# Performance work log

Measured on AMD Instinct MI355X. Metric: run time of the kernel, lower is better.

Reference implementation:

```python
import jax, jax.numpy as jnp
import numpy as np

B, T, D, H = 16, 2048, 512, 512


def setup_inputs() -> dict:
    key = jax.random.key(0)
    k1, k2, k3, k4, k5, k6 = jax.random.split(key, 6)
    s = 1.0 / np.sqrt(H)  # PyTorch RNN init scale
    return {
        "input_features": jax.random.normal(k1, (B, T, D), jnp.float32),
        "start_index": jax.random.randint(k2, (B,), 0, T),
        "w_ih": jax.random.uniform(k3, (3 * H, D), jnp.float32, -s, s),
        "w_hh": jax.random.uniform(k4, (3 * H, H), jnp.float32, -s, s),
        "b_ih": jax.random.uniform(k5, (3 * H,), jnp.float32, -s, s),
        "b_hh": jax.random.uniform(k6, (3 * H,), jnp.float32, -s, s),
    }


def reference(input_features, start_index, w_ih, w_hh, b_ih, b_hh):
    # Faithful to RNNSeqMaskEncoder._forward_residual with 1-layer uni GRU,
    # Identity residual (input_dim == hidden_dim), default_hidden == zeros.
    Bn, Tn, _ = input_features.shape
    Hn = w_hh.shape[1]
    dt = input_features.dtype
    # Precompute input projections for all timesteps: (B, T, 3H)
    x_proj = jnp.einsum('btd,gd->btg', input_features, w_ih) + b_ih
    # Mask at step i: keep hidden only if start_index < i (else reset to zeros).
    masks = (start_index[None, :] < jnp.arange(Tn)[:, None]).astype(dt)  # (T, B)

    def step(h, inp):
        xg, m = inp                     # xg: (B, 3H), m: (B,)
        h = h * m[:, None]              # mask-based hidden reset
        hg = h @ w_hh.T + b_hh          # (B, 3H)
        xr, xz, xn = jnp.split(xg, 3, axis=-1)
        hr, hz, hn = jnp.split(hg, 3, axis=-1)
        r = jax.nn.sigmoid(xr + hr)
        z = jax.nn.sigmoid(xz + hz)
        n = jnp.tanh(xn + r * hn)
        h_new = (1.0 - z) * n + z * h   # PyTorch GRU update
        return h_new, h_new

    h0 = jnp.zeros((Bn, Hn), dt)
    _, hs = jax.lax.scan(step, h0, (x_proj.transpose(1, 0, 2), masks))  # hs: (T, B, H)
    hidden_seq = hs.transpose(1, 0, 2)          # (B, T, H)
    output = input_features + hidden_seq        # residual (Identity linear)
    hidden = hidden_seq[None]                   # (n_layers*dirs=1, B, T, H)
    return output, hidden
```

## Files before the change

### kernel.cpp

```cpp
#include <hip/hip_runtime.h>
#include <cstdint>

typedef short bf16x8 __attribute__((ext_vector_type(8)));
typedef float f32x4  __attribute__((ext_vector_type(4)));
typedef unsigned u32x4 __attribute__((ext_vector_type(4)));

constexpr int Bn = 16, Tn = 2048, Dn = 512, Hn = 512;
constexpr int NWG = 16, JWG = 32, NTH = 512;
constexpr int NLAUNCH = 128;
constexpr int TC1 = 16;

#define MFMA16(a, b, c) __builtin_amdgcn_mfma_f32_16x16x32_bf16((a), (b), (c), 0, 0, 0)

#define POLLS_FAST() do { \
  asm volatile("global_load_dwordx4 %0, %1, off sc0 nt" : "=v"(a0) : "v"(hpF)      : "memory"); \
  asm volatile("global_load_dwordx4 %0, %1, off sc0 nt" : "=v"(a1) : "v"(hpF + 16) : "memory"); \
  asm volatile("global_load_dwordx4 %0, %1, off sc0 nt" : "=v"(a2) : "v"(hpF + 32) : "memory"); \
  asm volatile("global_load_dwordx4 %0, %1, off sc0 nt" : "=v"(a3) : "v"(hpF + 48) : "memory"); \
} while (0)
#define POLLS_SLOW() do { \
  asm volatile("global_load_dwordx4 %0, %1, off sc0 sc1" : "=v"(a0) : "v"(hpS)      : "memory"); \
  asm volatile("global_load_dwordx4 %0, %1, off sc0 sc1" : "=v"(a1) : "v"(hpS + 16) : "memory"); \
  asm volatile("global_load_dwordx4 %0, %1, off sc0 sc1" : "=v"(a2) : "v"(hpS + 32) : "memory"); \
  asm volatile("global_load_dwordx4 %0, %1, off sc0 sc1" : "=v"(a3) : "v"(hpS + 48) : "memory"); \
} while (0)
#define PUBS_PEND(slot_t) do { \
  if (!(jj & 1)) { \
    unsigned* dstS_ = ringS + (size_t)((slot_t) & 1) * (Bn * Hn / 2) + ((bq * Hn + jg) >> 1); \
    asm volatile("global_store_dword %0, %1, off sc0 sc1" :: "v"(dstS_), "v"(pendP) : "memory"); \
  } \
} while (0)

__device__ __forceinline__ unsigned short f2bf(float f) {
  union { float f; unsigned u; } v; v.f = f;
  unsigned r = v.u + 0x7FFFu + ((v.u >> 16) & 1u);
  return (unsigned short)(r >> 16);
}
__device__ __forceinline__ float lo2f(unsigned u) { union { unsigned u; float f; } v; v.u = u << 16;        return v.f; }
__device__ __forceinline__ float hi2f(unsigned u) { union { unsigned u; float f; } v; v.u = u & 0xFFFF0000u; return v.f; }
__device__ __forceinline__ float asf(unsigned u)  { union { unsigned u; float f; } v; v.u = u; return v.f; }
__device__ __forceinline__ unsigned asu(float f)  { union { float f; unsigned u; } v; v.f = f; return v.u; }

__global__ __launch_bounds__(NTH, 2) void xproj_pass(
    const float* __restrict__ x, const float* __restrict__ w_ih,
    const float* __restrict__ b_ih, const float* __restrict__ b_hh,
    unsigned* __restrict__ xrz, unsigned short* __restrict__ xnb)
{
  const int tid = threadIdx.x, lane = tid & 63, wv = tid >> 6;
  const int kw = wv & 3, jw = wv >> 2;
  const int arow = lane & 15, koff = (lane >> 4) * 8;
  const int wg = blockIdx.x, t0 = blockIdx.y * TC1;
  const int kb = kw * 128;

  bf16x8 wif[3][4];
  #pragma unroll
  for (int g = 0; g < 3; ++g) {
    const int grow = g * Hn + wg * JWG + jw * 16 + arow;
    #pragma unroll
    for (int s = 0; s < 4; ++s) {
      const float* pi = w_ih + (size_t)grow * Dn + kb + s * 32 + koff;
      bf16x8 b;
      #pragma unroll
      for (int i = 0; i < 8; ++i) b[i] = (short)f2bf(pi[i]);
      wif[g][s] = b;
    }
  }
  const int bq = tid >> 5, jj = tid & 31, jg = wg * JWG + jj;
  const float br = b_ih[jg]          + b_hh[jg];
  const float bz = b_ih[Hn + jg]     + b_hh[Hn + jg];
  const float bn = b_ih[2 * Hn + jg];

  __shared__ float red[3][4][16][32];
  const float* xrow = x + (size_t)arow * Tn * Dn + kb + koff;

  for (int tt = 0; tt < TC1; ++tt) {
    const int t = t0 + tt;
    const float* xt = xrow + (size_t)t * Dn;
    f32x4 xa[4][2];
    #pragma unroll
    for (int s = 0; s < 4; ++s) {
      xa[s][0] = *(const f32x4*)(xt + s * 32);
      xa[s][1] = *(const f32x4*)(xt + s * 32 + 4);
    }
    bf16x8 xf[4];
    #pragma unroll
    for (int s = 0; s < 4; ++s) {
      unsigned d0, d1, d2, d3;
      asm("v_cvt_pk_bf16_f32 %0, %1, %2" : "=v"(d0) : "v"(xa[s][0][0]), "v"(xa[s][0][1]));
      asm("v_cvt_pk_bf16_f32 %0, %1, %2" : "=v"(d1) : "v"(xa[s][0][2]), "v"(xa[s][0][3]));
      asm("v_cvt_pk_bf16_f32 %0, %1, %2" : "=v"(d2) : "v"(xa[s][1][0]), "v"(xa[s][1][1]));
      asm("v_cvt_pk_bf16_f32 %0, %1, %2" : "=v"(d3) : "v"(xa[s][1][2]), "v"(xa[s][1][3]));
      union { u32x4 u; bf16x8 v; } xu;
      xu.u[0] = d0; xu.u[1] = d1; xu.u[2] = d2; xu.u[3] = d3;
      xf[s] = xu.v;
    }
    f32x4 ar = {0,0,0,0}, az = {0,0,0,0}, an = {0,0,0,0};
    #pragma unroll
    for (int s = 0; s < 4; ++s) {
      ar = MFMA16(xf[s], wif[0][s], ar);
      az = MFMA16(xf[s], wif[1][s], az);
      an = MFMA16(xf[s], wif[2][s], an);
    }
    #pragma unroll
    for (int i = 0; i < 4; ++i) {
      const int r_ = (lane >> 4) * 4 + i, c_ = jw * 16 + (lane & 15);
      red[0][kw][r_][c_] = ar[i];
      red[1][kw][r_][c_] = az[i];
      red[2][kw][r_][c_] = an[i];
    }
    __syncthreads();
    float sr = br, sz = bz, sn = bn;
    #pragma unroll
    for (int k2 = 0; k2 < 4; ++k2) {
      sr += red[0][k2][bq][jj];
      sz += red[1][k2][bq][jj];
      sn += red[2][k2][bq][jj];
    }
    unsigned rz;
    asm("v_cvt_pk_bf16_f32 %0, %1, %2" : "=v"(rz) : "v"(sr), "v"(sz));
    const size_t o = (size_t)(wg * Tn + t) * 512 + tid;
    xrz[o] = rz;
    xnb[o] = f2bf(sn);
    __syncthreads();
  }
}

template<bool XP>
__global__ __launch_bounds__(NTH, 2) void gru_scan(
    const float* __restrict__ x, const int* __restrict__ start,
    const float* __restrict__ w_ih, const float* __restrict__ w_hh,
    const float* __restrict__ b_ih, const float* __restrict__ b_hh,
    float* __restrict__ out, unsigned* __restrict__ ectl,
    unsigned* __restrict__ ringF, unsigned* __restrict__ ringS,
    const unsigned* __restrict__ xrz, const unsigned short* __restrict__ xnb)
{
  __shared__ int s_rank;
  __shared__ int s_fastok;
  if (threadIdx.x == 0) {
    unsigned xcc;
    asm volatile("s_getreg_b32 %0, hwreg(HW_REG_XCC_ID)" : "=s"(xcc));
    xcc &= 7u;
    if (blockIdx.x == 0)
      __hip_atomic_store(&ectl[8], xcc | 0x100u, __ATOMIC_RELAXED, __HIP_MEMORY_SCOPE_AGENT);
    unsigned w;
    while ((((w = __hip_atomic_load(&ectl[8], __ATOMIC_RELAXED, __HIP_MEMORY_SCOPE_AGENT))) & 0x100u) == 0u)
      __builtin_amdgcn_s_sleep(2);
    if ((w & 7u) != xcc)
      for (int i = 0; i < 800; ++i) __builtin_amdgcn_s_sleep(2);
    const unsigned slot =
        __hip_atomic_fetch_add(&ectl[9], 1u, __ATOMIC_RELAXED, __HIP_MEMORY_SCOPE_AGENT);
    s_rank = (slot < (unsigned)NWG) ? (int)slot : -1;
  }
  __syncthreads();
  const int rank = s_rank;
  if (rank < 0) return;

  const int tid = threadIdx.x, lane = tid & 63, wv = tid >> 6;
  const int kw = wv & 3, jw = wv >> 2;
  const int arow = lane & 15, koff = (lane >> 4) * 8;
  const int kb = kw * 128;
  constexpr int NG = XP ? 3 : 4;

  bf16x8 whf[3][4], wif[3][4];
  #pragma unroll
  for (int g = 0; g < 3; ++g) {
    const int grow = g * Hn + rank * JWG + jw * 16 + arow;
    #pragma unroll
    for (int s = 0; s < 4; ++s) {
      const float* ph = w_hh + (size_t)grow * Dn + kb + s * 32 + koff;
      bf16x8 a;
      #pragma unroll
      for (int i = 0; i < 8; ++i) a[i] = (short)f2bf(ph[i]);
      whf[g][s] = a;
      if constexpr (!XP) {
        const float* pi = w_ih + (size_t)grow * Dn + kb + s * 32 + koff;
        bf16x8 b;
        #pragma unroll
        for (int i = 0; i < 8; ++i) b[i] = (short)f2bf(pi[i]);
        wif[g][s] = b;
      }
    }
  }

  if (threadIdx.x == 0) {
    if (rank == 0) {
      const unsigned* tp = &ectl[32];
      asm volatile("global_store_dword %0, %1, off" :: "v"(tp), "v"(0xA5A5A5A5u) : "memory");
      asm volatile("s_waitcnt vmcnt(0)" ::: "memory");
      __hip_atomic_store(&ectl[10], 1u, __ATOMIC_RELAXED, __HIP_MEMORY_SCOPE_AGENT);
    }
    while (__hip_atomic_load(&ectl[10], __ATOMIC_RELAXED, __HIP_MEMORY_SCOPE_AGENT) == 0u)
      __builtin_amdgcn_s_sleep(1);
    int ok = 0;
    const unsigned* tp = &ectl[32];
    for (int i = 0; i < 1024 && !ok; ++i) {
      unsigned tok;
      asm volatile("global_load_dword %0, %1, off sc0 nt" : "=v"(tok) : "v"(tp) : "memory");
      asm volatile("s_waitcnt vmcnt(0)" ::: "memory");
      ok = (tok == 0xA5A5A5A5u);
      if (!ok && (i & 15) == 15) __builtin_amdgcn_s_sleep(1);
    }
    s_fastok = ok;
    __hip_atomic_store(&ectl[64 + rank], 1u, __ATOMIC_RELAXED, __HIP_MEMORY_SCOPE_AGENT);
    for (;;) {
      unsigned rdy = 0;
      for (int i = 0; i < 16; ++i)
        rdy += __hip_atomic_load(&ectl[64 + i], __ATOMIC_RELAXED, __HIP_MEMORY_SCOPE_AGENT);
      if (rdy == 16u) break;
      __builtin_amdgcn_s_sleep(1);
    }
  }
  __syncthreads();
  bool fastwave = (s_fastok != 0);

  const int bq = tid >> 5, jj = tid & 31, jg = rank * JWG + jj;
  const float bias_nh = b_hh[2 * Hn + jg];
  float bias_r = 0.f, bias_z = 0.f, bias_nx = 0.f;
  if constexpr (!XP) {
    bias_r  = b_ih[jg]      + b_hh[jg];
    bias_z  = b_ih[Hn + jg] + b_hh[Hn + jg];
    bias_nx = b_ih[2 * Hn + jg];
  }
  const int start_g = start[bq];
  const int start_a = start[arow];
  const int jwr  = jj >> 4;
  const int lsrc = ((bq >> 2) << 4) | (jj & 15);
  const int ib   = bq & 3;

  float h_own = 0.f;
  unsigned po0u = 0u, po1u = 0u;
  unsigned pendP = 0u;
  __shared__ float red[2][NG][4][2][64][4];

  const float*          xres_p = x   + (size_t)bq * Tn * Dn + jg;
  const unsigned*       xrz_p  = xrz + (size_t)rank * Tn * 512 + tid;
  const unsigned short* xn_p   = xnb + (size_t)rank * Tn * 512 + tid;
  const float*          xrow   = x   + (size_t)arow * Tn * Dn + kb + koff;

  unsigned prz0=0, prz1=0, prz2=0, prz3=0, pn0=0, pn1=0, pn2=0, pn3=0;
  unsigned pxr0=0, pxr1=0, pxr2=0, pxr3=0;
  f32x4 xa0[4][2], xa1[4][2]; float xr0 = 0.f, xr1 = 0.f;
  if constexpr (XP) {
    prz0 = xrz_p[0];   pn0 = xn_p[0];
    prz1 = xrz_p[512]; pn1 = xn_p[512];
    pxr0 = asu(xres_p[0]); pxr1 = asu(xres_p[Dn]);
  } else {
    #pragma unroll
    for (int s = 0; s < 4; ++s) {
      xa0[s][0] = *(const f32x4*)(xrow + s * 32);
      xa0[s][1] = *(const f32x4*)(xrow + s * 32 + 4);
      xa1[s][0] = *(const f32x4*)(xrow + (size_t)Dn + s * 32);
      xa1[s][1] = *(const f32x4*)(xrow + (size_t)Dn + s * 32 + 4);
    }
    xr0 = xres_p[0]; xr1 = xres_p[Dn];
  }

  auto step = [&](int t, unsigned& crz, unsigned& cn, unsigned& cxr,
                  unsigned& frz, unsigned& fn, unsigned& fxr,
                  f32x4 (&xa)[4][2], float& xr) {
    const bool hv = (t > 0);
    const float xres_t = XP ? asf(cxr) : xr;
    f32x4 ar = {0,0,0,0}, az = {0,0,0,0}, anx = {0,0,0,0}, anh = {0,0,0,0};

    if constexpr (!XP) {
      bf16x8 xf[4];
      #pragma unroll
      for (int s = 0; s < 4; ++s) {
        unsigned d0, d1, d2, d3;
        asm("v_cvt_pk_bf16_f32 %0, %1, %2" : "=v"(d0) : "v"(xa[s][0][0]), "v"(xa[s][0][1]));
        asm("v_cvt_pk_bf16_f32 %0, %1, %2" : "=v"(d1) : "v"(xa[s][0][2]), "v"(xa[s][0][3]));
        asm("v_cvt_pk_bf16_f32 %0, %1, %2" : "=v"(d2) : "v"(xa[s][1][0]), "v"(xa[s][1][1]));
        asm("v_cvt_pk_bf16_f32 %0, %1, %2" : "=v"(d3) : "v"(xa[s][1][2]), "v"(xa[s][1][3]));
        union { u32x4 u; bf16x8 v; } xu;
        xu.u[0] = d0; xu.u[1] = d1; xu.u[2] = d2; xu.u[3] = d3;
        xf[s] = xu.v;
      }
      #pragma unroll
      for (int s = 0; s < 4; ++s) {
        ar  = MFMA16(xf[s], wif[0][s], ar);
        az  = MFMA16(xf[s], wif[1][s], az);
        anx = MFMA16(xf[s], wif[2][s], anx);
      }
    }

    const size_t off_h = (size_t)(t & 1) * (Bn * Hn / 2) + ((arow * Hn + kb + koff) >> 1);
    const unsigned* hpF = ringF + off_h;
    const unsigned* hpS = ringS + off_h;
    u32x4 a0, a1, a2, a3;
    if (hv) {
      if (!fastwave) PUBS_PEND(t);
      if (fastwave) POLLS_FAST(); else POLLS_SLOW();
      asm volatile("s_waitcnt vmcnt(0)" ::: "memory");
      __builtin_amdgcn_sched_barrier(0);
      const unsigned pexp = (unsigned)((t >> 1) & 1);
      int tries = 0;
      for (;;) {
        int ok;
        if (pexp) {
          const unsigned andv = a0[0] & a0[1] & a0[2] & a0[3] & a1[0] & a1[1] & a1[2] & a1[3]
                              & a2[0] & a2[1] & a2[2] & a2[3] & a3[0] & a3[1] & a3[2] & a3[3];
          ok = ((andv & 0x00010001u) == 0x00010001u);
        } else {
          const unsigned orv  = a0[0] | a0[1] | a0[2] | a0[3] | a1[0] | a1[1] | a1[2] | a1[3]
                              | a2[0] | a2[1] | a2[2] | a2[3] | a3[0] | a3[1] | a3[2] | a3[3];
          ok = ((orv & 0x00010001u) == 0u);
        }
        if (__all(ok)) break;
        ++tries;
        if (fastwave && tries >= 8192) {
          fastwave = false;
          PUBS_PEND(t);
        }
        if (!fastwave || tries > 32) __builtin_amdgcn_s_sleep(1);
        if (fastwave) POLLS_FAST(); else POLLS_SLOW();
        asm volatile("s_waitcnt vmcnt(0)" ::: "memory");
        __builtin_amdgcn_sched_barrier(0);
      }
    }

    if (hv) {
      const bool am = (start_a < t);
      union { u32x4 u; bf16x8 v; } c0, c1, c2, c3;
      const u32x4 zz = {0, 0, 0, 0};
      c0.u = am ? a0 : zz; c1.u = am ? a1 : zz; c2.u = am ? a2 : zz; c3.u = am ? a3 : zz;
      ar  = MFMA16(c0.v, whf[0][0], ar);  az  = MFMA16(c0.v, whf[1][0], az);
      anh = MFMA16(c0.v, whf[2][0], anh);
      ar  = MFMA16(c1.v, whf[0][1], ar);  az  = MFMA16(c1.v, whf[1][1], az);
      anh = MFMA16(c1.v, whf[2][1], anh);
      ar  = MFMA16(c2.v, whf[0][2], ar);  az  = MFMA16(c2.v, whf[1][2], az);
      anh = MFMA16(c2.v, whf[2][2], anh);
      ar  = MFMA16(c3.v, whf[0][3], ar);  az  = MFMA16(c3.v, whf[1][3], az);
      anh = MFMA16(c3.v, whf[2][3], anh);
    }

    const int par = t & 1;
    *(f32x4*)&red[par][0][kw][jw][lane][0] = ar;
    *(f32x4*)&red[par][1][kw][jw][lane][0] = az;
    if constexpr (XP) {
      *(f32x4*)&red[par][2][kw][jw][lane][0] = anh;
    } else {
      *(f32x4*)&red[par][2][kw][jw][lane][0] = anx;
      *(f32x4*)&red[par][3][kw][jw][lane][0] = anh;
    }
    __syncthreads();

    if constexpr (XP) {
      const int tf = (t + 2 < Tn) ? t + 2 : Tn - 1;
      const unsigned*       p1 = xrz_p + (size_t)tf * 512;
      const unsigned short* p2 = xn_p  + (size_t)tf * 512;
      const float*          p3 = xres_p + (size_t)tf * Dn;
      asm volatile("global_load_dword  %0, %1, off" : "=v"(frz) : "v"(p1) : "memory");
      asm volatile("global_load_ushort %0, %1, off" : "=v"(fn)  : "v"(p2) : "memory");
      asm volatile("global_load_dword  %0, %1, off" : "=v"(fxr) : "v"(p3) : "memory");
    } else {
      const int tf = (t + 2 < Tn) ? t + 2 : Tn - 1;
      const float* xt = xrow + (size_t)tf * Dn;
      #pragma unroll
      for (int s = 0; s < 4; ++s) {
        xa[s][0] = *(const f32x4*)(xt + s * 32);
        xa[s][1] = *(const f32x4*)(xt + s * 32 + 4);
      }
      xr = xres_p[(size_t)tf * Dn];
    }
    if (hv) {
      const size_t poo = ((size_t)bq * Tn + (t - 1)) * Hn + jg;
      const float* q0 = out + poo;
      const float* q1 = out + (size_t)Bn * Tn * Hn + poo;
      asm volatile("global_store_dword %0, %1, off" :: "v"(q0), "v"(po0u) : "memory");
      asm volatile("global_store_dword %0, %1, off" :: "v"(q1), "v"(po1u) : "memory");
    }
    if (hv && fastwave) PUBS_PEND(t);

    float sr, sz, snx, snh;
    if constexpr (XP) { sr = lo2f(crz); sz = hi2f(crz); snx = lo2f(cn); snh = bias_nh; }
    else              { sr = bias_r;    sz = bias_z;    snx = bias_nx;  snh = bias_nh; }
    #pragma unroll
    for (int k2 = 0; k2 < 4; ++k2) {
      sr += red[par][0][k2][jwr][lsrc][ib];
      sz += red[par][1][k2][jwr][lsrc][ib];
      if constexpr (XP) {
        snh += red[par][2][k2][jwr][lsrc][ib];
      } else {
        snx += red[par][2][k2][jwr][lsrc][ib];
        snh += red[par][3][k2][jwr][lsrc][ib];
      }
    }
    const float r  = 1.f / (1.f + __expf(-sr));
    const float z  = 1.f / (1.f + __expf(-sz));
    const float ea = __expf(2.f * (snx + r * snh));
    const float n  = 1.f - 2.f / (ea + 1.f);
    const float hm = (start_g < t) ? h_own : 0.f;
    const float hn = (1.f - z) * n + z * hm;
    h_own = hn;

    const unsigned ptag01 = (unsigned)(((t + 1) >> 1) & 1) * 0x00010001u;
    const float hpart = asf((unsigned)__shfl_xor((int)asu(hn), 1, 64));
    unsigned packed;
    asm("v_cvt_pk_bf16_f32 %0, %1, %2" : "=v"(packed) : "v"(hn), "v"(hpart));
    packed = (packed & 0xFFFEFFFEu) | ptag01;
    if (!(jj & 1)) {
      unsigned* dstF = ringF + (size_t)((t + 1) & 1) * (Bn * Hn / 2) + ((bq * Hn + jg) >> 1);
      asm volatile("global_store_dword %0, %1, off" :: "v"(dstF), "v"(packed) : "memory");
    }
    pendP = packed;

    po0u = asu(xres_t + hn);
    po1u = asu(hn);
  };

  #pragma unroll 1
  for (int t = 0; t < Tn; t += 4) {
    step(t + 0, prz0, pn0, pxr0, prz2, pn2, pxr2, xa0, xr0);
    step(t + 1, prz1, pn1, pxr1, prz3, pn3, pxr3, xa1, xr1);
    step(t + 2, prz2, pn2, pxr2, prz0, pn0, pxr0, xa0, xr0);
    step(t + 3, prz3, pn3, pxr3, prz1, pn1, pxr1, xa1, xr1);
  }
  {
    const size_t poo = ((size_t)bq * Tn + (Tn - 1)) * Hn + jg;
    out[poo] = asf(po0u);
    out[(size_t)Bn * Tn * Hn + poo] = asf(po1u);
  }
}

extern "C" void kernel_launch(void* const* d_in, const int* in_sizes, int n_in,
                              void* d_out, int out_size, void* d_ws, size_t ws_size,
                              hipStream_t stream) {
  const float* x     = (const float*)d_in[0];
  const int*   start = (const int*)d_in[1];
  const float* w_ih  = (const float*)d_in[2];
  const float* w_hh  = (const float*)d_in[3];
  const float* b_ih  = (const float*)d_in[4];
  const float* b_hh  = (const float*)d_in[5];
  float* out = (float*)d_out;

  unsigned* ectl  = (unsigned*)d_ws;
  unsigned* ringF = (unsigned*)((char*)d_ws + 4096);
  unsigned* ringS = (unsigned*)((char*)d_ws + 36864);
  const size_t xrz_off   = 131072;
  const size_t xrz_bytes = (size_t)NWG * Tn * 512 * 4;
  const size_t xn_bytes  = (size_t)NWG * Tn * 512 * 2;
  unsigned*       xrz = (unsigned*)((char*)d_ws + xrz_off);
  unsigned short* xnb = (unsigned short*)((char*)d_ws + xrz_off + xrz_bytes);
  const bool xp = ws_size >= xrz_off + xrz_bytes + xn_bytes;

  hipMemsetAsync(d_ws, 0x00, 4096, stream);
  hipMemsetAsync((char*)d_ws + 4096,  0x00, 16384, stream);
  hipMemsetAsync((char*)d_ws + 20480, 0x01, 16384, stream);
  hipMemsetAsync((char*)d_ws + 36864, 0x00, 16384, stream);
  hipMemsetAsync((char*)d_ws + 53248, 0x01, 16384, stream);
  if (xp) {
    hipLaunchKernelGGL(xproj_pass, dim3(NWG, Tn / TC1), dim3(NTH), 0, stream,
                       x, w_ih, b_ih, b_hh, xrz, xnb);
    hipLaunchKernelGGL(gru_scan<true>, dim3(NLAUNCH), dim3(NTH), 0, stream,
                       x, start, w_ih, w_hh, b_ih, b_hh, out, ectl, ringF, ringS, xrz, xnb);
  } else {
    hipLaunchKernelGGL(gru_scan<false>, dim3(NLAUNCH), dim3(NTH), 0, stream,
                       x, start, w_ih, w_hh, b_ih, b_hh, out, ectl, ringF, ringS,
                       (const unsigned*)d_ws, (const unsigned short*)d_ws);
  }
}
```

Baseline: 5.262 ms.

## Agree on fast path globally, reorder stores, and swizzle LDS reduction layout

All workgroups now agree once at startup whether the fast coherent ring path works, using an AND over per-rank flags. This replaces the per-wave fallback that republished to the slow ring, and each step now writes to exactly one ring. The output stores move ahead of the poll wait, which now waits with vmcnt(2) so the stores can stay in flight, and the MFMA and reduction block moves after the next-step prefetch loads. The LDS reduction buffer is laid out as [batch][column] with an XOR swizzle so reads are simple and avoid bank conflicts. The trade-off is the loss of a runtime fallback if the fast path stalls mid-run, which risks a hang.

Result: faster. 4.693 ms (-10.8%).

```diff
diff --git a/kernel.cpp b/kernel.cpp
--- a/kernel.cpp
+++ b/kernel.cpp
@@ -24,12 +24,6 @@
   asm volatile("global_load_dwordx4 %0, %1, off sc0 sc1" : "=v"(a2) : "v"(hpS + 32) : "memory"); \
   asm volatile("global_load_dwordx4 %0, %1, off sc0 sc1" : "=v"(a3) : "v"(hpS + 48) : "memory"); \
 } while (0)
-#define PUBS_PEND(slot_t) do { \
-  if (!(jj & 1)) { \
-    unsigned* dstS_ = ringS + (size_t)((slot_t) & 1) * (Bn * Hn / 2) + ((bq * Hn + jg) >> 1); \
-    asm volatile("global_store_dword %0, %1, off sc0 sc1" :: "v"(dstS_), "v"(pendP) : "memory"); \
-  } \
-} while (0)
 
 __device__ __forceinline__ unsigned short f2bf(float f) {
   union { float f; unsigned u; } v; v.f = f;
@@ -135,7 +129,7 @@
     const unsigned* __restrict__ xrz, const unsigned short* __restrict__ xnb)
 {
   __shared__ int s_rank;
-  __shared__ int s_fastok;
+  __shared__ int s_fast;
   if (threadIdx.x == 0) {
     unsigned xcc;
     asm volatile("s_getreg_b32 %0, hwreg(HW_REG_XCC_ID)" : "=s"(xcc));
@@ -200,18 +194,23 @@
       ok = (tok == 0xA5A5A5A5u);
       if (!ok && (i & 15) == 15) __builtin_amdgcn_s_sleep(1);
     }
-    s_fastok = ok;
-    __hip_atomic_store(&ectl[64 + rank], 1u, __ATOMIC_RELAXED, __HIP_MEMORY_SCOPE_AGENT);
+    __hip_atomic_store(&ectl[64 + rank], ok ? 1u : 2u, __ATOMIC_RELAXED, __HIP_MEMORY_SCOPE_AGENT);
+    unsigned andok;
     for (;;) {
-      unsigned rdy = 0;
-      for (int i = 0; i < 16; ++i)
-        rdy += __hip_atomic_load(&ectl[64 + i], __ATOMIC_RELAXED, __HIP_MEMORY_SCOPE_AGENT);
-      if (rdy == 16u) break;
+      andok = 1u;
+      unsigned done = 0;
+      for (int i = 0; i < 16; ++i) {
+        const unsigned v = __hip_atomic_load(&ectl[64 + i], __ATOMIC_RELAXED, __HIP_MEMORY_SCOPE_AGENT);
+        done += (v != 0u);
+        andok &= (v == 1u);
+      }
+      if (done == 16u) break;
       __builtin_amdgcn_s_sleep(1);
     }
+    s_fast = (int)andok;
   }
   __syncthreads();
-  bool fastwave = (s_fastok != 0);
+  const bool fast = (s_fast != 0);
 
   const int bq = tid >> 5, jj = tid & 31, jg = rank * JWG + jj;
   const float bias_nh = b_hh[2 * Hn + jg];
@@ -223,14 +222,11 @@
   }
   const int start_g = start[bq];
   const int start_a = start[arow];
-  const int jwr  = jj >> 4;
-  const int lsrc = ((bq >> 2) << 4) | (jj & 15);
-  const int ib   = bq & 3;
+  const int jr = jj ^ (((bq >> 2) & 1) << 4);
 
   float h_own = 0.f;
   unsigned po0u = 0u, po1u = 0u;
-  unsigned pendP = 0u;
-  __shared__ float red[2][NG][4][2][64][4];
+  __shared__ float red[2][NG][4][16][32];
 
   const float*          xres_p = x   + (size_t)bq * Tn * Dn + jg;
   const unsigned*       xrz_p  = xrz + (size_t)rank * Tn * 512 + tid;
@@ -288,9 +284,16 @@
     const unsigned* hpS = ringS + off_h;
     u32x4 a0, a1, a2, a3;
     if (hv) {
-      if (!fastwave) PUBS_PEND(t);
-      if (fastwave) POLLS_FAST(); else POLLS_SLOW();
-      asm volatile("s_waitcnt vmcnt(0)" ::: "memory");
+      if (fast) POLLS_FAST(); else POLLS_SLOW();
+      {
+        const size_t poo = ((size_t)bq * Tn + (t - 1)) * Hn + jg;
+        const float* q0 = out + poo;
+        const float* q1 = out + (size_t)Bn * Tn * Hn + poo;
+        asm volatile("global_store_dword %0, %1, off" :: "v"(q0), "v"(po0u) : "memory");
+        asm volatile("global_store_dword %0, %1, off" :: "v"(q1), "v"(po1u) : "memory");
+      }
+      if (fast) { asm volatile("s_waitcnt vmcnt(2)" ::: "memory"); }
+      else      { asm volatile("s_waitcnt vmcnt(0)" ::: "memory"); }
       __builtin_amdgcn_sched_barrier(0);
       const unsigned pexp = (unsigned)((t >> 1) & 1);
       int tries = 0;
@@ -307,42 +310,12 @@
         }
         if (__all(ok)) break;
         ++tries;
-        if (fastwave && tries >= 8192) {
-          fastwave = false;
-          PUBS_PEND(t);
-        }
-        if (!fastwave || tries > 32) __builtin_amdgcn_s_sleep(1);
-        if (fastwave) POLLS_FAST(); else POLLS_SLOW();
+        if (!fast || tries > 32) __builtin_amdgcn_s_sleep(1);
+        if (fast) POLLS_FAST(); else POLLS_SLOW();
         asm volatile("s_waitcnt vmcnt(0)" ::: "memory");
         __builtin_amdgcn_sched_barrier(0);
       }
     }
-
-    if (hv) {
-      const bool am = (start_a < t);
-      union { u32x4 u; bf16x8 v; } c0, c1, c2, c3;
-      const u32x4 zz = {0, 0, 0, 0};
-      c0.u = am ? a0 : zz; c1.u = am ? a1 : zz; c2.u = am ? a2 : zz; c3.u = am ? a3 : zz;
-      ar  = MFMA16(c0.v, whf[0][0], ar);  az  = MFMA16(c0.v, whf[1][0], az);
-      anh = MFMA16(c0.v, whf[2][0], anh);
-      ar  = MFMA16(c1.v, whf[0][1], ar);  az  = MFMA16(c1.v, whf[1][1], az);
-      anh = MFMA16(c1.v, whf[2][1], anh);
-      ar  = MFMA16(c2.v, whf[0][2], ar);  az  = MFMA16(c2.v, whf[1][2], az);
-      anh = MFMA16(c2.v, whf[2][2], anh);
-      ar  = MFMA16(c3.v, whf[0][3], ar);  az  = MFMA16(c3.v, whf[1][3], az);
-      anh = MFMA16(c3.v, whf[2][3], anh);
-    }
-
-    const int par = t & 1;
-    *(f32x4*)&red[par][0][kw][jw][lane][0] = ar;
-    *(f32x4*)&red[par][1][kw][jw][lane][0] = az;
-    if constexpr (XP) {
-      *(f32x4*)&red[par][2][kw][jw][lane][0] = anh;
-    } else {
-      *(f32x4*)&red[par][2][kw][jw][lane][0] = anx;
-      *(f32x4*)&red[par][3][kw][jw][lane][0] = anh;
-    }
-    __syncthreads();
 
     if constexpr (XP) {
       const int tf = (t + 2 < Tn) ? t + 2 : Tn - 1;
@@ -362,27 +335,49 @@
       }
       xr = xres_p[(size_t)tf * Dn];
     }
+
     if (hv) {
-      const size_t poo = ((size_t)bq * Tn + (t - 1)) * Hn + jg;
-      const float* q0 = out + poo;
-      const float* q1 = out + (size_t)Bn * Tn * Hn + poo;
-      asm volatile("global_store_dword %0, %1, off" :: "v"(q0), "v"(po0u) : "memory");
-      asm volatile("global_store_dword %0, %1, off" :: "v"(q1), "v"(po1u) : "memory");
-    }
-    if (hv && fastwave) PUBS_PEND(t);
-
+      const bool am = (start_a < t);
+      union { u32x4 u; bf16x8 v; } c0, c1, c2, c3;
+      const u32x4 zz = {0, 0, 0, 0};
+      c0.u = am ? a0 : zz; c1.u = am ? a1 : zz; c2.u = am ? a2 : zz; c3.u = am ? a3 : zz;
+      ar  = MFMA16(c0.v, whf[0][0], ar);  az  = MFMA16(c0.v, whf[1][0], az);
+      anh = MFMA16(c0.v, whf[2][0], anh);
+      ar  = MFMA16(c1.v, whf[0][1], ar);  az  = MFMA16(c1.v, whf[1][1], az);
+      anh = MFMA16(c1.v, whf[2][1], anh);
+      ar  = MFMA16(c2.v, whf[0][2], ar);  az  = MFMA16(c2.v, whf[1][2], az);
+      anh = MFMA16(c2.v, whf[2][2], anh);
+      ar  = MFMA16(c3.v, whf[0][3], ar);  az  = MFMA16(c3.v, whf[1][3], az);
+      anh = MFMA16(c3.v, whf[2][3], anh);
+    }
+
+    const int par = t & 1;
+    #pragma unroll
+    for (int i = 0; i < 4; ++i) {
+      const int r_ = (lane >> 4) * 4 + i;
+      const int c_ = (jw * 16 + (lane & 15)) ^ (((lane >> 4) & 1) << 4);
+      red[par][0][kw][r_][c_] = ar[i];
+      red[par][1][kw][r_][c_] = az[i];
+      if constexpr (XP) {
+        red[par][2][kw][r_][c_] = anh[i];
+      } else {
+        red[par][2][kw][r_][c_] = anx[i];
+        red[par][3][kw][r_][c_] = anh[i];
+      }
+    }
+    __syncthreads();
     float sr, sz, snx, snh;
     if constexpr (XP) { sr = lo2f(crz); sz = hi2f(crz); snx = lo2f(cn); snh = bias_nh; }
     else              { sr = bias_r;    sz = bias_z;    snx = bias_nx;  snh = bias_nh; }
     #pragma unroll
     for (int k2 = 0; k2 < 4; ++k2) {
-      sr += red[par][0][k2][jwr][lsrc][ib];
-      sz += red[par][1][k2][jwr][lsrc][ib];
+      sr += red[par][0][k2][bq][jr];
+      sz += red[par][1][k2][bq][jr];
       if constexpr (XP) {
-        snh += red[par][2][k2][jwr][lsrc][ib];
+        snh += red[par][2][k2][bq][jr];
       } else {
-        snx += red[par][2][k2][jwr][lsrc][ib];
-        snh += red[par][3][k2][jwr][lsrc][ib];
+        snx += red[par][2][k2][bq][jr];
+        snh += red[par][3][k2][bq][jr];
       }
     }
     const float r  = 1.f / (1.f + __expf(-sr));
@@ -399,10 +394,15 @@
     asm("v_cvt_pk_bf16_f32 %0, %1, %2" : "=v"(packed) : "v"(hn), "v"(hpart));
     packed = (packed & 0xFFFEFFFEu) | ptag01;
     if (!(jj & 1)) {
-      unsigned* dstF = ringF + (size_t)((t + 1) & 1) * (Bn * Hn / 2) + ((bq * Hn + jg) >> 1);
-      asm volatile("global_store_dword %0, %1, off" :: "v"(dstF), "v"(packed) : "memory");
-    }
-    pendP = packed;
+      const size_t doff = (size_t)((t + 1) & 1) * (Bn * Hn / 2) + ((bq * Hn + jg) >> 1);
+      if (fast) {
+        unsigned* dstF = ringF + doff;
+        asm volatile("global_store_dword %0, %1, off" :: "v"(dstF), "v"(packed) : "memory");
+      } else {
+        unsigned* dstS = ringS + doff;
+        asm volatile("global_store_dword %0, %1, off sc0 sc1" :: "v"(dstS), "v"(packed) : "memory");
+      }
+    }
 
     po0u = asu(xres_t + hn);
     po1u = asu(hn);
```
